# Kernel tuning notes

Measured on AMD Instinct MI355X. Metric: run time of the kernel, lower is better.

## Reference

```python
import jax, jax.numpy as jnp
import numpy as np

R = 0.8      # jet radius used to normalize pairwise distances
BETA = 1.0   # EMD angular exponent (matches beta=1.0 in emd()/emd_loss default)


def setup_inputs() -> dict:
    key = jax.random.key(0)
    k1, k2, k3, k4 = jax.random.split(key, 4)
    Ni, Nj, D = 6144, 6144, 2   # event points, shape-sample points, (eta, phi)
    M, K = 1024, 256            # batched simplex projection: rows x components
    y_i = jax.random.normal(k1, (Ni, D), dtype=jnp.float32)
    y_j = jax.random.normal(k2, (Nj, D), dtype=jnp.float32)
    x = jax.random.uniform(k3, (Ni, Nj), dtype=jnp.float32)
    x_ij = x / jnp.sum(x)       # transport plan normalized to unit total mass
    f = jax.random.normal(k4, (M, K), dtype=jnp.float32)
    return {"y_i": y_i, "y_j": y_j, "x_ij": x_ij, "f": f}


def _activate(f):
    # Euclidean projection of each row of f onto the probability simplex
    # (sort descending -> running threshold -> relu shift), as in activate().
    m, n = f.shape
    u = jnp.sort(f, axis=1)[:, ::-1]                                   # [m, n] descending
    v = (jnp.cumsum(u, axis=1) - 1.0) / jnp.arange(1, n + 1, dtype=f.dtype)
    rho = jnp.sum((u > v).astype(jnp.int32), axis=1) - 1               # [m]
    w = jnp.take_along_axis(v, rho[:, None], axis=1)                   # [m, 1]
    return jax.nn.relu(f - w)


def _emd_loss(y_i, y_j, x_ij):
    # theta_ij = sum_d | ((y_i - y_j) / R)^beta |  ; loss = sum theta_ij * x_ij
    diff = (y_i[:, None, :] - y_j[None, :, :]) / R                     # [Ni, Nj, D]
    theta = jnp.sum(jnp.abs(diff ** BETA), axis=-1)                    # [Ni, Nj]
    return jnp.sum(theta * x_ij)


def reference(y_i, y_j, x_ij, f):
    loss = _emd_loss(y_i, y_j, x_ij)   # scalar EMD-style transport loss
    z_proj = _activate(f)              # [M, K] simplex-projected weights
    return (loss, z_proj)
```

## Files before the change

kernel.cpp:

```cpp
#include <hip/hip_runtime.h>

#define NI 6144
#define NJ 6144
#define M_ROWS 1024
#define K_COLS 256
#define ROWS_PER_BLOCK 8
#define EMD_BLOCKS (NI / ROWS_PER_BLOCK)

__global__ __launch_bounds__(256) void emd_partial_kernel(
    const float* __restrict__ y_i, const float* __restrict__ y_j,
    const float* __restrict__ x, float* __restrict__ partial) {
  __shared__ float4 yj0v[NJ / 4];
  __shared__ float4 yj1v[NJ / 4];
  {
    const float4* yj4 = (const float4*)y_j;
    float* s0 = (float*)yj0v;
    float* s1 = (float*)yj1v;
    for (int t = threadIdx.x; t < NJ / 2; t += 256) {
      const float4 v = yj4[t];
      s0[2 * t]     = v.x;  s1[2 * t]     = v.y;
      s0[2 * t + 1] = v.z;  s1[2 * t + 1] = v.w;
    }
  }
  __syncthreads();

  const int row0 = blockIdx.x * ROWS_PER_BLOCK;
  float yi0[ROWS_PER_BLOCK], yi1[ROWS_PER_BLOCK];
#pragma unroll
  for (int r = 0; r < ROWS_PER_BLOCK; ++r) {
    yi0[r] = y_i[2 * (row0 + r)];
    yi1[r] = y_i[2 * (row0 + r) + 1];
  }

  float acc = 0.0f;
#pragma unroll
  for (int t = 0; t < NJ / 4 / 256; ++t) {
    const int idx = threadIdx.x + t * 256;
    const float4 ya = yj0v[idx];
    const float4 yb = yj1v[idx];
#pragma unroll
    for (int r = 0; r < ROWS_PER_BLOCK; ++r) {
      const float4 xv =
          ((const float4*)(x + (size_t)(row0 + r) * NJ))[idx];
      acc += xv.x * (fabsf(yi0[r] - ya.x) + fabsf(yi1[r] - yb.x));
      acc += xv.y * (fabsf(yi0[r] - ya.y) + fabsf(yi1[r] - yb.y));
      acc += xv.z * (fabsf(yi0[r] - ya.z) + fabsf(yi1[r] - yb.z));
      acc += xv.w * (fabsf(yi0[r] - ya.w) + fabsf(yi1[r] - yb.w));
    }
  }

  for (int off = 32; off > 0; off >>= 1) acc += __shfl_down(acc, off, 64);
  __shared__ float wsum[4];
  const int lane = threadIdx.x & 63;
  const int wid = threadIdx.x >> 6;
  if (lane == 0) wsum[wid] = acc;
  __syncthreads();
  if (threadIdx.x == 0)
    partial[blockIdx.x] = wsum[0] + wsum[1] + wsum[2] + wsum[3];
}

__global__ __launch_bounds__(256) void simplex_and_finish_kernel(
    const float* __restrict__ f, const float* __restrict__ partial,
    float* __restrict__ out) {
  const int tid = threadIdx.x;
  const int lane = tid & 63;
  const int wid = tid >> 6;

  __shared__ float s[K_COLS];
  __shared__ float wpre[4];

  if (blockIdx.x == M_ROWS) {
    float acc = partial[tid] + partial[tid + 256] + partial[tid + 512];
    for (int off = 32; off > 0; off >>= 1) acc += __shfl_down(acc, off, 64);
    if (lane == 0) wpre[wid] = acc;
    __syncthreads();
    if (tid == 0)
      out[0] = (wpre[0] + wpre[1] + wpre[2] + wpre[3]) * 1.25f;
    return;
  }

  const int row = blockIdx.x;
  const float fv = f[row * K_COLS + tid];

  float x = fv;
#pragma unroll
  for (int k = 2; k <= 64; k <<= 1) {
#pragma unroll
    for (int j = k >> 1; j > 0; j >>= 1) {
      const float pv = __shfl_xor(x, j, 64);
      const bool up = ((tid & k) == 0);
      const bool lower = ((tid & j) == 0);
      x = (up == lower) ? fmaxf(x, pv) : fminf(x, pv);
    }
  }
  {
    s[tid] = x; __syncthreads();
    const float pv = s[tid ^ 64]; __syncthreads();
    const bool up = ((tid & 128) == 0);
    x = (up == ((tid & 64) == 0)) ? fmaxf(x, pv) : fminf(x, pv);
#pragma unroll
    for (int j = 32; j > 0; j >>= 1) {
      const float pv2 = __shfl_xor(x, j, 64);
      x = (up == ((tid & j) == 0)) ? fmaxf(x, pv2) : fminf(x, pv2);
    }
  }
  {
    s[tid] = x; __syncthreads();
    float pv = s[tid ^ 128]; __syncthreads();
    x = ((tid & 128) == 0) ? fmaxf(x, pv) : fminf(x, pv);
    s[tid] = x; __syncthreads();
    pv = s[tid ^ 64]; __syncthreads();
    x = ((tid & 64) == 0) ? fmaxf(x, pv) : fminf(x, pv);
#pragma unroll
    for (int j = 32; j > 0; j >>= 1) {
      const float pv2 = __shfl_xor(x, j, 64);
      x = ((tid & j) == 0) ? fmaxf(x, pv2) : fminf(x, pv2);
    }
  }

  const float u = x;

  float cs = u;
#pragma unroll
  for (int off = 1; off < 64; off <<= 1) {
    const float t = __shfl_up(cs, off, 64);
    if (lane >= off) cs += t;
  }
  if (lane == 63) wpre[wid] = cs;
  __syncthreads();
  float base = 0.0f;
#pragma unroll
  for (int w = 0; w < 4; ++w)
    if (w < wid) base += wpre[w];
  cs += base;

  const float vt = (cs - 1.0f) / (float)(tid + 1);
  s[tid] = vt;
  const int cnt = __syncthreads_count(u > vt);
  const float w = s[cnt - 1];

  out[1 + row * K_COLS + tid] = fmaxf(fv - w, 0.0f);
}

extern "C" void kernel_launch(void* const* d_in, const int* in_sizes, int n_in,
                              void* d_out, int out_size, void* d_ws,
                              size_t ws_size, hipStream_t stream) {
  const float* y_i = (const float*)d_in[0];
  const float* y_j = (const float*)d_in[1];
  const float* x   = (const float*)d_in[2];
  const float* f   = (const float*)d_in[3];
  float* out = (float*)d_out;
  float* partial = (float*)d_ws;

  emd_partial_kernel<<<EMD_BLOCKS, 256, 0, stream>>>(y_i, y_j, x, partial);
  simplex_and_finish_kernel<<<M_ROWS + 1, 256, 0, stream>>>(f, partial, out);
}
```

Measured before the change: 227.6 us.

## Fuse EMD partial and simplex projection into one launch, read y_j from global

Merges the EMD partial-sum blocks and the per-row simplex projection blocks into a single heterogeneous kernel, so the simplex work runs alongside the bandwidth-bound EMD pass. The final scalar reduction moves into a small separate finish kernel. The 48KB shared-memory staging of y_j is dropped in favour of direct float4 global (cached) loads, which frees LDS and should raise occupancy, with a launch-bounds hint of 4 blocks per CU. In exchange, every EMD block re-reads y_j through the cache, and register pressure may rise under the launch bound.

```diff
diff --git a/kernel.cpp b/kernel.cpp
--- a/kernel.cpp
+++ b/kernel.cpp
@@ -6,119 +6,93 @@
 #define K_COLS 256
 #define ROWS_PER_BLOCK 8
 #define EMD_BLOCKS (NI / ROWS_PER_BLOCK)
+#define TOTAL_BLOCKS (EMD_BLOCKS + M_ROWS)
 
-__global__ __launch_bounds__(256) void emd_partial_kernel(
+__global__ __launch_bounds__(256, 4) void fused_kernel(
     const float* __restrict__ y_i, const float* __restrict__ y_j,
-    const float* __restrict__ x, float* __restrict__ partial) {
-  __shared__ float4 yj0v[NJ / 4];
-  __shared__ float4 yj1v[NJ / 4];
-  {
-    const float4* yj4 = (const float4*)y_j;
-    float* s0 = (float*)yj0v;
-    float* s1 = (float*)yj1v;
-    for (int t = threadIdx.x; t < NJ / 2; t += 256) {
-      const float4 v = yj4[t];
-      s0[2 * t]     = v.x;  s1[2 * t]     = v.y;
-      s0[2 * t + 1] = v.z;  s1[2 * t + 1] = v.w;
-    }
-  }
-  __syncthreads();
-
-  const int row0 = blockIdx.x * ROWS_PER_BLOCK;
-  float yi0[ROWS_PER_BLOCK], yi1[ROWS_PER_BLOCK];
-#pragma unroll
-  for (int r = 0; r < ROWS_PER_BLOCK; ++r) {
-    yi0[r] = y_i[2 * (row0 + r)];
-    yi1[r] = y_i[2 * (row0 + r) + 1];
-  }
-
-  float acc = 0.0f;
-#pragma unroll
-  for (int t = 0; t < NJ / 4 / 256; ++t) {
-    const int idx = threadIdx.x + t * 256;
-    const float4 ya = yj0v[idx];
-    const float4 yb = yj1v[idx];
-#pragma unroll
-    for (int r = 0; r < ROWS_PER_BLOCK; ++r) {
-      const float4 xv =
-          ((const float4*)(x + (size_t)(row0 + r) * NJ))[idx];
-      acc += xv.x * (fabsf(yi0[r] - ya.x) + fabsf(yi1[r] - yb.x));
-      acc += xv.y * (fabsf(yi0[r] - ya.y) + fabsf(yi1[r] - yb.y));
-      acc += xv.z * (fabsf(yi0[r] - ya.z) + fabsf(yi1[r] - yb.z));
-      acc += xv.w * (fabsf(yi0[r] - ya.w) + fabsf(yi1[r] - yb.w));
-    }
-  }
-
-  for (int off = 32; off > 0; off >>= 1) acc += __shfl_down(acc, off, 64);
-  __shared__ float wsum[4];
-  const int lane = threadIdx.x & 63;
-  const int wid = threadIdx.x >> 6;
-  if (lane == 0) wsum[wid] = acc;
-  __syncthreads();
-  if (threadIdx.x == 0)
-    partial[blockIdx.x] = wsum[0] + wsum[1] + wsum[2] + wsum[3];
-}
-
-__global__ __launch_bounds__(256) void simplex_and_finish_kernel(
-    const float* __restrict__ f, const float* __restrict__ partial,
-    float* __restrict__ out) {
+    const float* __restrict__ x, const float* __restrict__ f,
+    float* __restrict__ partial, float* __restrict__ out) {
+  __shared__ float s[K_COLS];
+  __shared__ float wpre[4];
   const int tid = threadIdx.x;
   const int lane = tid & 63;
   const int wid = tid >> 6;
 
-  __shared__ float s[K_COLS];
-  __shared__ float wpre[4];
+  if (blockIdx.x < EMD_BLOCKS) {
+    const int row0 = blockIdx.x * ROWS_PER_BLOCK;
+    float yi0[ROWS_PER_BLOCK], yi1[ROWS_PER_BLOCK];
+#pragma unroll
+    for (int r = 0; r < ROWS_PER_BLOCK; ++r) {
+      yi0[r] = y_i[2 * (row0 + r)];
+      yi1[r] = y_i[2 * (row0 + r) + 1];
+    }
 
-  if (blockIdx.x == M_ROWS) {
-    float acc = partial[tid] + partial[tid + 256] + partial[tid + 512];
+    const float4* yj4 = (const float4*)y_j;
+    float acc = 0.0f;
+#pragma unroll
+    for (int t = 0; t < NJ / 4 / 256; ++t) {
+      const int idx = tid + t * 256;
+      const float4 p = yj4[2 * idx];
+      const float4 q = yj4[2 * idx + 1];
+#pragma unroll
+      for (int r = 0; r < ROWS_PER_BLOCK; ++r) {
+        const float4 xv =
+            ((const float4*)(x + (size_t)(row0 + r) * NJ))[idx];
+        acc += xv.x * (fabsf(yi0[r] - p.x) + fabsf(yi1[r] - p.y));
+        acc += xv.y * (fabsf(yi0[r] - p.z) + fabsf(yi1[r] - p.w));
+        acc += xv.z * (fabsf(yi0[r] - q.x) + fabsf(yi1[r] - q.y));
+        acc += xv.w * (fabsf(yi0[r] - q.z) + fabsf(yi1[r] - q.w));
+      }
+    }
+
     for (int off = 32; off > 0; off >>= 1) acc += __shfl_down(acc, off, 64);
     if (lane == 0) wpre[wid] = acc;
     __syncthreads();
     if (tid == 0)
-      out[0] = (wpre[0] + wpre[1] + wpre[2] + wpre[3]) * 1.25f;
+      partial[blockIdx.x] = wpre[0] + wpre[1] + wpre[2] + wpre[3];
     return;
   }
 
-  const int row = blockIdx.x;
+  const int row = blockIdx.x - EMD_BLOCKS;
   const float fv = f[row * K_COLS + tid];
 
-  float x = fv;
+  float xs = fv;
 #pragma unroll
   for (int k = 2; k <= 64; k <<= 1) {
 #pragma unroll
     for (int j = k >> 1; j > 0; j >>= 1) {
-      const float pv = __shfl_xor(x, j, 64);
+      const float pv = __shfl_xor(xs, j, 64);
       const bool up = ((tid & k) == 0);
       const bool lower = ((tid & j) == 0);
-      x = (up == lower) ? fmaxf(x, pv) : fminf(x, pv);
+      xs = (up == lower) ? fmaxf(xs, pv) : fminf(xs, pv);
     }
   }
   {
-    s[tid] = x; __syncthreads();
+    s[tid] = xs; __syncthreads();
     const float pv = s[tid ^ 64]; __syncthreads();
     const bool up = ((tid & 128) == 0);
-    x = (up == ((tid & 64) == 0)) ? fmaxf(x, pv) : fminf(x, pv);
+    xs = (up == ((tid & 64) == 0)) ? fmaxf(xs, pv) : fminf(xs, pv);
 #pragma unroll
     for (int j = 32; j > 0; j >>= 1) {
-      const float pv2 = __shfl_xor(x, j, 64);
-      x = (up == ((tid & j) == 0)) ? fmaxf(x, pv2) : fminf(x, pv2);
+      const float pv2 = __shfl_xor(xs, j, 64);
+      xs = (up == ((tid & j) == 0)) ? fmaxf(xs, pv2) : fminf(xs, pv2);
     }
   }
   {
-    s[tid] = x; __syncthreads();
+    s[tid] = xs; __syncthreads();
     float pv = s[tid ^ 128]; __syncthreads();
-    x = ((tid & 128) == 0) ? fmaxf(x, pv) : fminf(x, pv);
-    s[tid] = x; __syncthreads();
+    xs = ((tid & 128) == 0) ? fmaxf(xs, pv) : fminf(xs, pv);
+    s[tid] = xs; __syncthreads();
     pv = s[tid ^ 64]; __syncthreads();
-    x = ((tid & 64) == 0) ? fmaxf(x, pv) : fminf(x, pv);
+    xs = ((tid & 64) == 0) ? fmaxf(xs, pv) : fminf(xs, pv);
 #pragma unroll
     for (int j = 32; j > 0; j >>= 1) {
-      const float pv2 = __shfl_xor(x, j, 64);
-      x = ((tid & j) == 0) ? fmaxf(x, pv2) : fminf(x, pv2);
+      const float pv2 = __shfl_xor(xs, j, 64);
+      xs = ((tid & j) == 0) ? fmaxf(xs, pv2) : fminf(xs, pv2);
     }
   }
 
-  const float u = x;
+  const float u = xs;
 
   float cs = u;
 #pragma unroll
@@ -142,6 +116,20 @@
   out[1 + row * K_COLS + tid] = fmaxf(fv - w, 0.0f);
 }
 
+__global__ __launch_bounds__(256) void finish_kernel(
+    const float* __restrict__ partial, float* __restrict__ out) {
+  const int tid = threadIdx.x;
+  const int lane = tid & 63;
+  const int wid = tid >> 6;
+  __shared__ float wpre[4];
+  float acc = partial[tid] + partial[tid + 256] + partial[tid + 512];
+  for (int off = 32; off > 0; off >>= 1) acc += __shfl_down(acc, off, 64);
+  if (lane == 0) wpre[wid] = acc;
+  __syncthreads();
+  if (tid == 0)
+    out[0] = (wpre[0] + wpre[1] + wpre[2] + wpre[3]) * 1.25f;
+}
+
 extern "C" void kernel_launch(void* const* d_in, const int* in_sizes, int n_in,
                               void* d_out, int out_size, void* d_ws,
                               size_t ws_size, hipStream_t stream) {
@@ -152,6 +140,6 @@
   float* out = (float*)d_out;
   float* partial = (float*)d_ws;
 
-  emd_partial_kernel<<<EMD_BLOCKS, 256, 0, stream>>>(y_i, y_j, x, partial);
-  simplex_and_finish_kernel<<<M_ROWS + 1, 256, 0, stream>>>(f, partial, out);
+  fused_kernel<<<TOTAL_BLOCKS, 256, 0, stream>>>(y_i, y_j, x, f, partial, out);
+  finish_kernel<<<1, 256, 0, stream>>>(partial, out);
 }
```

New measurement: 220.6 us. 1.03x faster.
